# Kernel optimization log

Measured on AMD Instinct MI355X. Metric: run time of the kernel, lower is better.

The kernel has to match this reference:

```python
import jax, jax.numpy as jnp
import numpy as np

SIZE = 256
D_IN = 256
EPS = 1e-3  # keras BatchNormalization default epsilon


def _mlp(x, W1, b1, W2, b2):
    # smallMLP: Dense(size, relu) -> Dense(size)
    return jax.nn.relu(x @ W1 + b1) @ W2 + b2


def setup_inputs() -> dict:
    key = jax.random.key(0)
    ks = jax.random.split(key, 20)
    B, L1, L2 = 16, 1024, 1024
    s = 0.02
    inp = {
        "seq1M": jax.random.normal(ks[0], (B, L1, D_IN), jnp.float32),
        "seq2M": jax.random.normal(ks[1], (B, L2, D_IN), jnp.float32),
        "distogram": jax.random.uniform(ks[2], (B, L1, L2), jnp.float32),
        # shared K/Q/V smallMLP params (same layers applied to seq1 and seq2)
        "kW1": jax.random.normal(ks[3], (D_IN, SIZE), jnp.float32) * s,
        "kb1": jnp.zeros((SIZE,), jnp.float32),
        "kW2": jax.random.normal(ks[4], (SIZE, SIZE), jnp.float32) * s,
        "kb2": jnp.zeros((SIZE,), jnp.float32),
        "qW1": jax.random.normal(ks[5], (D_IN, SIZE), jnp.float32) * s,
        "qb1": jnp.zeros((SIZE,), jnp.float32),
        "qW2": jax.random.normal(ks[6], (SIZE, SIZE), jnp.float32) * s,
        "qb2": jnp.zeros((SIZE,), jnp.float32),
        "vW1": jax.random.normal(ks[7], (D_IN, SIZE), jnp.float32) * s,
        "vb1": jnp.zeros((SIZE,), jnp.float32),
        "vW2": jax.random.normal(ks[8], (SIZE, SIZE), jnp.float32) * s,
        "vb2": jnp.zeros((SIZE,), jnp.float32),
        # output projections
        "fc1W": jax.random.normal(ks[9], (SIZE, SIZE), jnp.float32) * s,
        "fc1b": jnp.zeros((SIZE,), jnp.float32),
        "fc2W": jax.random.normal(ks[10], (SIZE, SIZE), jnp.float32) * s,
        "fc2b": jnp.zeros((SIZE,), jnp.float32),
        # shared BatchNorm (inference mode, moving stats)
        "bn_gamma": jnp.ones((SIZE,), jnp.float32),
        "bn_beta": jnp.zeros((SIZE,), jnp.float32),
        "bn_mean": jnp.zeros((SIZE,), jnp.float32),
        "bn_var": jnp.ones((SIZE,), jnp.float32),
    }
    return inp


def reference(seq1M, seq2M, distogram,
              kW1, kb1, kW2, kb2,
              qW1, qb1, qW2, qb2,
              vW1, vb1, vW2, vb2,
              fc1W, fc1b, fc2W, fc2b,
              bn_gamma, bn_beta, bn_mean, bn_var):
    size = jnp.float32(SIZE)
    k1 = _mlp(seq1M, kW1, kb1, kW2, kb2)   # [B, L1, S]
    q1 = _mlp(seq1M, qW1, qb1, qW2, qb2)
    v1 = _mlp(seq1M, vW1, vb1, vW2, vb2)
    k2 = _mlp(seq2M, kW1, kb1, kW2, kb2)   # [B, L2, S]
    q2 = _mlp(seq2M, qW1, qb1, qW2, qb2)
    v2 = _mlp(seq2M, vW1, vb1, vW2, vb2)

    # distogram-scaled scores, softmax over axis 1 (query axis — non-standard)
    scores1 = jnp.einsum('bls,bms->blm', q1, k2) * distogram / size  # [B, L1, L2]
    w1 = jax.nn.softmax(scores1, axis=1)
    scores2 = jnp.einsum('bms,bls->bml', q2, k1) * jnp.transpose(distogram, (0, 2, 1)) / size  # [B, L2, L1]
    w2 = jax.nn.softmax(scores2, axis=1)

    # transpose(matmul(V^T, W), [0,2,1]) == einsum contracting the softmax axis
    ap1 = jnp.einsum('bls,blm->bms', v1, w1)  # [B, L2, S]
    ap2 = jnp.einsum('bms,bml->bls', v2, w2)  # [B, L1, S]

    def bn(x):
        return (x - bn_mean) * jax.lax.rsqrt(bn_var + EPS) * bn_gamma + bn_beta

    out1 = bn(jax.nn.relu(ap1 @ fc1W + fc1b))
    out2 = bn(jax.nn.relu(ap2 @ fc2W + fc2b))
    return out1, out2
```

## Files before the change

### kernel.cpp

```cpp
#include <hip/hip_runtime.h>
#include <hip/hip_bf16.h>


typedef __attribute__((ext_vector_type(8))) short bf16x8;
typedef __attribute__((ext_vector_type(4))) float f32x4;
typedef unsigned short u16;

__device__ __forceinline__ unsigned int f2bfbits(float f) {
  union { float f; unsigned int i; } v; v.f = f;
  return (v.i + 0x7fffu + ((v.i >> 16) & 1u)) >> 16;
}
__device__ __forceinline__ unsigned int pk2(float a, float b) {
  return f2bfbits(a) | (f2bfbits(b) << 16);
}
__device__ __forceinline__ float bf2f(u16 x) {
  union { unsigned int i; float f; } v;
  v.i = (unsigned int)x << 16;
  return v.f;
}

__global__ void pack_wt(const float* __restrict__ w0, const float* __restrict__ w1,
                        const float* __restrict__ w2, const float* __restrict__ w3,
                        const float* __restrict__ w4, const float* __restrict__ w5,
                        const float* __restrict__ w6, const float* __restrict__ w7,
                        u16* __restrict__ out) {
  const float* wsel[8] = {w0, w1, w2, w3, w4, w5, w6, w7};
  const float* W = wsel[blockIdx.y];
  u16* o = out + (size_t)blockIdx.y * 65536;
  int i0 = blockIdx.x * 1024 + threadIdx.x * 4;
  int n = i0 >> 8, k = i0 & 255;
  float a = W[(k + 0) * 256 + n];
  float b = W[(k + 1) * 256 + n];
  float c = W[(k + 2) * 256 + n];
  float d = W[(k + 3) * 256 + n];
  uint2 pv;
  pv.x = pk2(a, b);
  pv.y = pk2(c, d);
  *(uint2*)(o + i0) = pv;
}

__global__ __launch_bounds__(256, 2)
void mlp3_plus(const float* __restrict__ seqA, const float* __restrict__ seqB,
               const u16* __restrict__ Wt8,
               const float* __restrict__ kb1, const float* __restrict__ kb2,
               const float* __restrict__ qb1, const float* __restrict__ qb2,
               const float* __restrict__ vb1, const float* __restrict__ vb2,
               u16* __restrict__ kA, u16* __restrict__ qA, u16* __restrict__ vA,
               u16* __restrict__ kB, u16* __restrict__ qB, u16* __restrict__ vB,
               const float* __restrict__ D, u16* __restrict__ Dt)
{
  __shared__ union {
    struct {
      u16 As[64][256];
      u16 Hl[64][256];
    } m;
    u16 T[64][72];
  } sh;

  const int tid = threadIdx.x;

  if (blockIdx.x >= 512) {
    const int pb = blockIdx.x - 512;
    const int m0 = (pb & 15) * 64;
    const int l0 = ((pb >> 4) & 15) * 64;
    const int b = pb >> 8;
    const float* src = D + (size_t)b * (1024 * 1024);
    u16* dst = Dt + (size_t)b * (1024 * 1024);
    const int r = tid >> 2, c0 = (tid & 3) * 16;
    float4 f[4];
#pragma unroll
    for (int q = 0; q < 4; ++q)
      f[q] = *(const float4*)(src + (size_t)(l0 + r) * 1024 + m0 + c0 + q * 4);
    uint4 p0, p1;
    p0.x = pk2(f[0].x, f[0].y); p0.y = pk2(f[0].z, f[0].w);
    p0.z = pk2(f[1].x, f[1].y); p0.w = pk2(f[1].z, f[1].w);
    p1.x = pk2(f[2].x, f[2].y); p1.y = pk2(f[2].z, f[2].w);
    p1.z = pk2(f[3].x, f[3].y); p1.w = pk2(f[3].z, f[3].w);
    *(uint4*)&sh.T[r][c0] = p0;
    *(uint4*)&sh.T[r][c0 + 8] = p1;
    __syncthreads();
    u16 vals[16];
#pragma unroll
    for (int k = 0; k < 16; ++k) vals[k] = sh.T[c0 + k][r];
    *(uint4*)(dst + (size_t)(m0 + r) * 1024 + l0 + c0) = *(uint4*)&vals[0];
    *(uint4*)(dst + (size_t)(m0 + r) * 1024 + l0 + c0 + 8) = *(uint4*)&vals[8];
    return;
  }

  const int lane = tid & 63;
  const int w = tid >> 6;
  const int l15 = lane & 15, lq = lane >> 4;
  const int seqsel = blockIdx.x >> 8;
  const size_t m0 = (size_t)(blockIdx.x & 255) * 64;
  const float* __restrict__ seq = seqsel ? seqB : seqA;

  {
    const int row = tid >> 2, cg = tid & 3;
    const float* src = seq + (m0 + row) * 256 + cg * 64;
#pragma unroll
    for (int cc = 0; cc < 8; ++cc) {
      float4 f0 = *(const float4*)(src + cc * 8);
      float4 f1 = *(const float4*)(src + cc * 8 + 4);
      uint4 pk;
      pk.x = pk2(f0.x, f0.y);
      pk.y = pk2(f0.z, f0.w);
      pk.z = pk2(f1.x, f1.y);
      pk.w = pk2(f1.z, f1.w);
      const int ch = (cg * 8 + cc) ^ (row & 7);
      *(uint4*)&sh.m.As[row][ch * 8] = pk;
    }
  }
  __syncthreads();

  for (int mlp = 0; mlp < 3; ++mlp) {
    const u16* __restrict__ W1 = Wt8 + (size_t)(mlp * 2) * 65536;
    const u16* __restrict__ W2 = W1 + 65536;
    const float* __restrict__ b1 = (mlp == 0) ? kb1 : (mlp == 1) ? qb1 : vb1;
    const float* __restrict__ b2 = (mlp == 0) ? kb2 : (mlp == 1) ? qb2 : vb2;
    u16* __restrict__ dst =
        (mlp == 0) ? (seqsel ? kB : kA) : (mlp == 1) ? (seqsel ? qB : qA) : (seqsel ? vB : vA);

    const u16* __restrict__ w1b = W1 + (size_t)(w * 64 + l15) * 256 + lq * 8;
    const u16* __restrict__ w2b = W2 + (size_t)(w * 64 + l15) * 256 + lq * 8;

    bf16x8 wf[3][4];
#pragma unroll
    for (int ni = 0; ni < 4; ++ni) wf[0][ni] = *(const bf16x8*)(w1b + ni * 4096);
#pragma unroll
    for (int ni = 0; ni < 4; ++ni) wf[1][ni] = *(const bf16x8*)(w1b + ni * 4096 + 32);

    float b1v[4][4];
#pragma unroll
    for (int ni = 0; ni < 4; ++ni)
#pragma unroll
      for (int r = 0; r < 4; ++r) b1v[ni][r] = b1[w * 64 + ni * 16 + 4 * lq + r];
    float b2v[4];
#pragma unroll
    for (int ni = 0; ni < 4; ++ni) b2v[ni] = b2[w * 64 + ni * 16 + l15];

    f32x4 a1[4][4];
#pragma unroll
    for (int ni = 0; ni < 4; ++ni)
#pragma unroll
      for (int mj = 0; mj < 4; ++mj) a1[ni][mj] = (f32x4)0.0f;
#pragma unroll
    for (int ks = 0; ks < 8; ++ks) {
      if (ks + 2 < 8) {
#pragma unroll
        for (int ni = 0; ni < 4; ++ni)
          wf[(ks + 2) % 3][ni] = *(const bf16x8*)(w1b + ni * 4096 + (ks + 2) * 32);
      }
      bf16x8 af[4];
#pragma unroll
      for (int mj = 0; mj < 4; ++mj) {
        const int row = mj * 16 + l15;
        const int ch = (ks * 4 + lq) ^ (row & 7);
        af[mj] = *(const bf16x8*)&sh.m.As[row][ch * 8];
      }
#pragma unroll
      for (int ni = 0; ni < 4; ++ni)
#pragma unroll
        for (int mj = 0; mj < 4; ++mj)
          a1[ni][mj] = __builtin_amdgcn_mfma_f32_16x16x32_bf16(
              wf[ks % 3][ni], af[mj], a1[ni][mj], 0, 0, 0);
    }

    __syncthreads();

#pragma unroll
    for (int ni = 0; ni < 4; ++ni) wf[0][ni] = *(const bf16x8*)(w2b + ni * 4096);
#pragma unroll
    for (int ni = 0; ni < 4; ++ni) wf[1][ni] = *(const bf16x8*)(w2b + ni * 4096 + 32);

#pragma unroll
    for (int ni = 0; ni < 4; ++ni) {
      const int chl = w * 8 + ni * 2 + (lq >> 1);
#pragma unroll
      for (int mj = 0; mj < 4; ++mj) {
        const int m = mj * 16 + l15;
        float h0 = fmaxf(a1[ni][mj][0] + b1v[ni][0], 0.f);
        float h1 = fmaxf(a1[ni][mj][1] + b1v[ni][1], 0.f);
        float h2 = fmaxf(a1[ni][mj][2] + b1v[ni][2], 0.f);
        float h3 = fmaxf(a1[ni][mj][3] + b1v[ni][3], 0.f);
        uint2 pv;
        pv.x = pk2(h0, h1);
        pv.y = pk2(h2, h3);
        const int ch = chl ^ (m & 7);
        *(uint2*)&sh.m.Hl[m][ch * 8 + (lq & 1) * 4] = pv;
      }
    }
    __syncthreads();

    f32x4 a2[4][4];
#pragma unroll
    for (int mi = 0; mi < 4; ++mi)
#pragma unroll
      for (int ni = 0; ni < 4; ++ni) a2[mi][ni] = (f32x4)0.0f;
#pragma unroll
    for (int ks = 0; ks < 8; ++ks) {
      if (ks + 2 < 8) {
#pragma unroll
        for (int ni = 0; ni < 4; ++ni)
          wf[(ks + 2) % 3][ni] = *(const bf16x8*)(w2b + ni * 4096 + (ks + 2) * 32);
      }
      bf16x8 hf[4];
#pragma unroll
      for (int mi = 0; mi < 4; ++mi) {
        const int row = mi * 16 + l15;
        const int ch = (ks * 4 + lq) ^ (row & 7);
        hf[mi] = *(const bf16x8*)&sh.m.Hl[row][ch * 8];
      }
#pragma unroll
      for (int mi = 0; mi < 4; ++mi)
#pragma unroll
        for (int ni = 0; ni < 4; ++ni)
          a2[mi][ni] = __builtin_amdgcn_mfma_f32_16x16x32_bf16(
              hf[mi], wf[ks % 3][ni], a2[mi][ni], 0, 0, 0);
    }

#pragma unroll
    for (int ni = 0; ni < 4; ++ni) {
      const int col = w * 64 + ni * 16 + l15;
      const float bb = b2v[ni];
#pragma unroll
      for (int mi = 0; mi < 4; ++mi) {
        const size_t grow0 = m0 + mi * 16 + 4 * lq;
        float z[4];
#pragma unroll
        for (int r = 0; r < 4; ++r) z[r] = a2[mi][ni][r] + bb;
        if (mlp != 2) {
#pragma unroll
          for (int r = 0; r < 4; ++r)
            dst[(grow0 + r) * 256 + col] = (u16)f2bfbits(z[r]);
        } else {
          uint2 pv;
          pv.x = pk2(z[0], z[1]);
          pv.y = pk2(z[2], z[3]);
          const size_t bb2 = grow0 >> 10, lrow = grow0 & 1023;
          *(uint2*)(dst + ((size_t)bb2 * 256 + col) * 1024 + lrow) = pv;
        }
      }
    }
  }
}

__global__ __launch_bounds__(256, 2)
void gemm_bn2(const u16* __restrict__ ap1, const u16* __restrict__ ap2,
              const u16* __restrict__ Wt8,
              const float* __restrict__ fc1b, const float* __restrict__ fc2b,
              float* __restrict__ out1, float* __restrict__ out2,
              const float* __restrict__ bn_g, const float* __restrict__ bn_b,
              const float* __restrict__ bn_m, const float* __restrict__ bn_v)
{
  __shared__ u16 As[128][64];
  __shared__ u16 Ws[64][64];
  const int tid = threadIdx.x;
  const int lane = tid & 63;
  const int w = tid >> 6;
  const int wr = w >> 1, wc = w & 1;
  const int l15 = lane & 15, lq = lane >> 4;
  const size_t bm = (size_t)blockIdx.x * 128;
  const int bn = blockIdx.y * 64;
  const int which = blockIdx.z;

  const u16* __restrict__ A0 = which ? ap2 : ap1;
  const u16* __restrict__ Wt = Wt8 + (size_t)(6 + which) * 65536;
  const float* __restrict__ bias = which ? fc2b : fc1b;
  float* __restrict__ Cout = which ? out2 : out1;

  const int sar = tid >> 1, sah = tid & 1;
  const int swr = tid >> 2, swc = tid & 3;

  f32x4 acc[4][2];
#pragma unroll
  for (int mi = 0; mi < 4; ++mi)
#pragma unroll
    for (int ni = 0; ni < 2; ++ni) acc[mi][ni] = (f32x4)0.0f;

  for (int k0 = 0; k0 < 256; k0 += 64) {
    __syncthreads();
    {
      const u16* A = A0 + (bm + sar) * 256 + k0 + sah * 32;
#pragma unroll
      for (int c = 0; c < 4; ++c) {
        uint4 v = *(const uint4*)(A + c * 8);
        int cc = (sah * 4 + c) ^ (sar & 7);
        *(uint4*)&As[sar][cc * 8] = v;
      }
    }
    {
      const u16* Wp = Wt + (size_t)(bn + swr) * 256 + k0 + swc * 16;
#pragma unroll
      for (int c = 0; c < 2; ++c) {
        uint4 v = *(const uint4*)(Wp + c * 8);
        int cc = (swc * 2 + c) ^ (swr & 7);
        *(uint4*)&Ws[swr][cc * 8] = v;
      }
    }
    __syncthreads();
#pragma unroll
    for (int ks = 0; ks < 2; ++ks) {
      bf16x8 af[4], wf[2];
#pragma unroll
      for (int mi = 0; mi < 4; ++mi) {
        int row = wr * 64 + mi * 16 + l15;
        int cc = (ks * 4 + lq) ^ (row & 7);
        af[mi] = *(const bf16x8*)&As[row][cc * 8];
      }
#pragma unroll
      for (int ni = 0; ni < 2; ++ni) {
        int row = wc * 32 + ni * 16 + l15;
        int cc = (ks * 4 + lq) ^ (row & 7);
        wf[ni] = *(const bf16x8*)&Ws[row][cc * 8];
      }
#pragma unroll
      for (int mi = 0; mi < 4; ++mi)
#pragma unroll
        for (int ni = 0; ni < 2; ++ni)
          acc[mi][ni] = __builtin_amdgcn_mfma_f32_16x16x32_bf16(
              af[mi], wf[ni], acc[mi][ni], 0, 0, 0);
    }
  }

#pragma unroll
  for (int ni = 0; ni < 2; ++ni) {
    const int col = bn + wc * 32 + ni * 16 + l15;
    const float bi = bias[col];
    const float g = bn_g[col];
    const float be = bn_b[col];
    const float mu = bn_m[col];
    const float iv = rsqrtf(bn_v[col] + 1e-3f);
#pragma unroll
    for (int mi = 0; mi < 4; ++mi) {
      const size_t grow0 = bm + wr * 64 + mi * 16 + 4 * lq;
#pragma unroll
      for (int r = 0; r < 4; ++r) {
        float z = acc[mi][ni][r] + bi;
        float zz = fmaxf(z, 0.f);
        Cout[(grow0 + r) * 256 + col] = (zz - mu) * iv * g + be;
      }
    }
  }
}

__global__ __launch_bounds__(512, 2)
void attn_mfma(const u16* __restrict__ Qa, const u16* __restrict__ Ka,
               const u16* __restrict__ Va, u16* __restrict__ OutA,
               const u16* __restrict__ Qb, const u16* __restrict__ Kb,
               const u16* __restrict__ Vb, u16* __restrict__ OutB,
               const u16* __restrict__ D1t, const float* __restrict__ D2)
{
  __shared__ union U {
    struct {
      u16 Ks[2][64][256];
      u16 Vts[2][256][64];
      u16 Pl[128][72];
    } s;
    u16 Osw[8][16][264];
  } u;

  const int orig = blockIdx.x;
  const int lid = (orig & 7) * 32 + (orig >> 3);
  const int dir = lid >> 7;
  const int b = (lid >> 3) & 15;
  const int i0 = (lid & 7) * 128;

  const u16* __restrict__ Q = dir ? Qb : Qa;
  const u16* __restrict__ K = dir ? Kb : Ka;
  const u16* __restrict__ Vt = dir ? Vb : Va;
  u16* __restrict__ Out = dir ? OutB : OutA;

  const int tid = threadIdx.x;
  const int lane = tid & 63;
  const int w = tid >> 6;
  const int l15 = lane & 15, lq = lane >> 4;
  const size_t sbase = (size_t)b * (1024 * 256);
  const size_t vtbase = (size_t)b * (256 * 1024);
  const size_t dbase = (size_t)b * (1024 * 1024);

  bf16x8 q[8];
  {
    const u16* Qp = Q + sbase + (size_t)(i0 + w * 16 + l15) * 256 + lq * 8;
#pragma unroll
    for (int ks = 0; ks < 8; ++ks) q[ks] = *(const bf16x8*)(Qp + ks * 32);
  }

  const int cb0 = w * 4;
  auto stage_K = [&](int bi, int j0) {
#pragma unroll
    for (int i = 0; i < 4; ++i) {
      const int cb = cb0 + i;
      const int krow = cb * 2 + (lane >> 5);
      const int kch = (lane & 31) ^ (krow & 7);
      const u16* gs = K + sbase + (size_t)(j0 + krow) * 256 + kch * 8;
      __builtin_amdgcn_global_load_lds(
          (const __attribute__((address_space(1))) unsigned int*)gs,
          (__attribute__((address_space(3))) unsigned int*)&u.s.Ks[bi][cb * 2][0],
          16, 0, 0);
    }
  };
  auto stage_V = [&](int bi, int j0) {
#pragma unroll
    for (int i = 0; i < 4; ++i) {
      const int cb = cb0 + i;
      const int vrow = cb * 8 + (lane >> 3);
      const int vch = lane & 7;
      const u16* gs = Vt + vtbase + (size_t)vrow * 1024 + j0 + ((vch ^ (vrow & 7)) * 8);
      __builtin_amdgcn_global_load_lds(
          (const __attribute__((address_space(1))) unsigned int*)gs,
          (__attribute__((address_space(3))) unsigned int*)&u.s.Vts[bi][cb * 8][0],
          16, 0, 0);
    }
  };

  float mrow[4], lsum[4];
  f32x4 o[16];
#pragma unroll
  for (int r = 0; r < 4; ++r) { mrow[r] = -1e30f; lsum[r] = 0.f; }
#pragma unroll
  for (int nt = 0; nt < 16; ++nt) o[nt] = (f32x4)0.0f;

  stage_K(0, 0);
  stage_V(0, 0);

  for (int t = 0; t < 16; ++t) {
    const int bi = t & 1;
    const int j0 = t * 64;

    u16 bregu[16];
    float bregf[16];
    if (dir == 0) {
#pragma unroll
      for (int nt = 0; nt < 4; ++nt)
#pragma unroll
        for (int r = 0; r < 4; ++r)
          bregu[nt * 4 + r] =
              D1t[dbase + (size_t)(i0 + w * 16 + 4 * lq + r) * 1024 + j0 + l15 + 16 * nt];
    } else {
#pragma unroll
      for (int nt = 0; nt < 4; ++nt)
#pragma unroll
        for (int r = 0; r < 4; ++r)
          bregf[nt * 4 + r] =
              D2[dbase + (size_t)(i0 + w * 16 + 4 * lq + r) * 1024 + j0 + l15 + 16 * nt];
    }

    if (t + 1 < 16) {
      stage_V(bi ^ 1, j0 + 64);
      stage_K(bi ^ 1, j0 + 64);
      asm volatile("s_waitcnt vmcnt(24)" ::: "memory");
    } else {
      asm volatile("s_waitcnt vmcnt(16)" ::: "memory");
    }
    __builtin_amdgcn_s_barrier();
    __builtin_amdgcn_sched_barrier(0);

    f32x4 sa[4];
#pragma unroll
    for (int nt = 0; nt < 4; ++nt) sa[nt] = (f32x4)0.0f;
    __builtin_amdgcn_s_setprio(1);
#pragma unroll
    for (int ks = 0; ks < 8; ++ks)
#pragma unroll
      for (int nt = 0; nt < 4; ++nt) {
        const int row = nt * 16 + l15;
        const int cc = (ks * 4 + lq) ^ (row & 7);
        bf16x8 kb = *(const bf16x8*)&u.s.Ks[bi][row][cc * 8];
        sa[nt] = __builtin_amdgcn_mfma_f32_16x16x32_bf16(q[ks], kb, sa[nt], 0, 0, 0);
      }
    __builtin_amdgcn_s_setprio(0);

    float s[4][4];
    bool need = false;
#pragma unroll
    for (int r = 0; r < 4; ++r)
#pragma unroll
      for (int nt = 0; nt < 4; ++nt) {
        const float bb = (dir == 0) ? bf2f(bregu[nt * 4 + r]) : bregf[nt * 4 + r];
        s[r][nt] = sa[nt][r] * bb * 0.00390625f;
        need = need || (s[r][nt] > mrow[r] + 8.f);
      }
    if (__any(need)) {
#pragma unroll
      for (int r = 0; r < 4; ++r) {
        float mx = fmaxf(fmaxf(s[r][0], s[r][1]), fmaxf(s[r][2], s[r][3]));
        mx = fmaxf(mx, __shfl_xor(mx, 1, 16));
        mx = fmaxf(mx, __shfl_xor(mx, 2, 16));
        mx = fmaxf(mx, __shfl_xor(mx, 4, 16));
        mx = fmaxf(mx, __shfl_xor(mx, 8, 16));
        const float mn = fmaxf(mrow[r], mx);
        const float sc = __expf(mrow[r] - mn);
        mrow[r] = mn;
        lsum[r] *= sc;
#pragma unroll
        for (int nt = 0; nt < 16; ++nt) o[nt][r] *= sc;
      }
    }
#pragma unroll
    for (int r = 0; r < 4; ++r) {
      const int qrow = w * 16 + 4 * lq + r;
#pragma unroll
      for (int nt = 0; nt < 4; ++nt) {
        const float p = __expf(s[r][nt] - mrow[r]);
        lsum[r] += p;
        u.s.Pl[qrow][nt * 16 + l15] = (u16)f2bfbits(p);
      }
    }
    asm volatile("s_waitcnt lgkmcnt(0)" ::: "memory");
    __builtin_amdgcn_sched_barrier(0);
    const bf16x8 pa0 = *(const bf16x8*)&u.s.Pl[w * 16 + l15][lq * 8];
    const bf16x8 pa1 = *(const bf16x8*)&u.s.Pl[w * 16 + l15][32 + lq * 8];

    __builtin_amdgcn_s_setprio(1);
#pragma unroll
    for (int nt = 0; nt < 16; ++nt) {
      const int row = nt * 16 + l15;
      const int cc0 = (0 * 4 + lq) ^ (row & 7);
      const int cc1 = (1 * 4 + lq) ^ (row & 7);
      bf16x8 vb0 = *(const bf16x8*)&u.s.Vts[bi][row][cc0 * 8];
      bf16x8 vb1 = *(const bf16x8*)&u.s.Vts[bi][row][cc1 * 8];
      o[nt] = __builtin_amdgcn_mfma_f32_16x16x32_bf16(pa0, vb0, o[nt], 0, 0, 0);
      o[nt] = __builtin_amdgcn_mfma_f32_16x16x32_bf16(pa1, vb1, o[nt], 0, 0, 0);
    }
    __builtin_amdgcn_s_setprio(0);

    asm volatile("s_waitcnt lgkmcnt(0)" ::: "memory");
    __builtin_amdgcn_s_barrier();
  }

  float inv[4];
#pragma unroll
  for (int r = 0; r < 4; ++r) {
    float rs = lsum[r];
    rs += __shfl_xor(rs, 1, 16);
    rs += __shfl_xor(rs, 2, 16);
    rs += __shfl_xor(rs, 4, 16);
    rs += __shfl_xor(rs, 8, 16);
    inv[r] = 1.0f / rs;
  }
  __builtin_amdgcn_s_barrier();
#pragma unroll
  for (int nt = 0; nt < 16; ++nt) {
#pragma unroll
    for (int r = 0; r < 4; ++r)
      u.Osw[w][4 * lq + r][nt * 16 + l15] = (u16)f2bfbits(o[nt][r] * inv[r]);
  }
  asm volatile("s_waitcnt lgkmcnt(0)" ::: "memory");
  __builtin_amdgcn_sched_barrier(0);
  {
    const int orow = lane >> 2, och = (lane & 3) * 64;
    const u16* src = &u.Osw[w][orow][och];
    u16* dst = Out + sbase + (size_t)(i0 + w * 16 + orow) * 256 + och;
#pragma unroll
    for (int c = 0; c < 8; ++c) *(uint4*)(dst + c * 8) = *(const uint4*)(src + c * 8);
  }
}

extern "C" void kernel_launch(void* const* d_in, const int* in_sizes, int n_in,
                              void* d_out, int out_size, void* d_ws, size_t ws_size,
                              hipStream_t stream)
{
  (void)in_sizes; (void)n_in; (void)out_size; (void)ws_size;

  const float* seq1  = (const float*)d_in[0];
  const float* seq2  = (const float*)d_in[1];
  const float* disto = (const float*)d_in[2];
  const float* kW1 = (const float*)d_in[3];
  const float* kb1 = (const float*)d_in[4];
  const float* kW2 = (const float*)d_in[5];
  const float* kb2 = (const float*)d_in[6];
  const float* qW1 = (const float*)d_in[7];
  const float* qb1 = (const float*)d_in[8];
  const float* qW2 = (const float*)d_in[9];
  const float* qb2 = (const float*)d_in[10];
  const float* vW1 = (const float*)d_in[11];
  const float* vb1 = (const float*)d_in[12];
  const float* vW2 = (const float*)d_in[13];
  const float* vb2 = (const float*)d_in[14];
  const float* fc1W = (const float*)d_in[15];
  const float* fc1b = (const float*)d_in[16];
  const float* fc2W = (const float*)d_in[17];
  const float* fc2b = (const float*)d_in[18];
  const float* bn_g = (const float*)d_in[19];
  const float* bn_b = (const float*)d_in[20];
  const float* bn_m = (const float*)d_in[21];
  const float* bn_v = (const float*)d_in[22];

  char* ws = (char*)d_ws;
  const size_t MB = 1024 * 1024;
  u16* Wt8 = (u16*)(ws);
  u16* k1  = (u16*)(ws + 1 * MB);
  u16* q1  = (u16*)(ws + 9 * MB);
  u16* k2  = (u16*)(ws + 17 * MB);
  u16* q2  = (u16*)(ws + 25 * MB);
  u16* v1t = (u16*)(ws + 33 * MB);
  u16* v2t = (u16*)(ws + 41 * MB);
  u16* ap1 = (u16*)(ws + 49 * MB);
  u16* ap2 = (u16*)(ws + 57 * MB);
  u16* D1t = (u16*)(ws + 65 * MB);

  pack_wt<<<dim3(64, 8), 256, 0, stream>>>(kW1, kW2, qW1, qW2, vW1, vW2, fc1W, fc2W, Wt8);

  mlp3_plus<<<dim3(4608), dim3(256), 0, stream>>>(
      seq1, seq2, Wt8, kb1, kb2, qb1, qb2, vb1, vb2,
      k1, q1, v1t, k2, q2, v2t, disto, D1t);

  attn_mfma<<<dim3(256), dim3(512), 0, stream>>>(
      k2, q1, v1t, ap1,
      k1, q2, v2t, ap2,
      D1t, disto);

  float* out1 = (float*)d_out;
  float* out2 = (float*)d_out + 4194304;
  gemm_bn2<<<dim3(128, 4, 2), dim3(256), 0, stream>>>(
      ap1, ap2, Wt8, fc1b, fc2b, out1, out2, bn_g, bn_b, bn_m, bn_v);
}
```

Before: 161.3 us.

## Fuse output FC projection, ReLU and BatchNorm into attention kernel epilogue

Removes the separate gemm_bn2 kernel. Each attention warp now reads its normalized 16x256 output tile from LDS as MFMA A-fragments and multiplies it by the FC weight matrix, loaded straight from global memory with one-step register prefetch. It then applies bias, ReLU and BatchNorm and writes fp32 results directly. This drops the bf16 ap1/ap2 round trip through memory and one kernel launch. In exchange, the attention kernel's tail gets longer, every warp reloads the full 256x256 weights from global/L2 without LDS sharing, and register pressure rises.

```diff
diff --git a/kernel.cpp b/kernel.cpp
--- a/kernel.cpp
+++ b/kernel.cpp
@@ -244,111 +244,17 @@
   }
 }
 
-__global__ __launch_bounds__(256, 2)
-void gemm_bn2(const u16* __restrict__ ap1, const u16* __restrict__ ap2,
-              const u16* __restrict__ Wt8,
-              const float* __restrict__ fc1b, const float* __restrict__ fc2b,
-              float* __restrict__ out1, float* __restrict__ out2,
-              const float* __restrict__ bn_g, const float* __restrict__ bn_b,
-              const float* __restrict__ bn_m, const float* __restrict__ bn_v)
-{
-  __shared__ u16 As[128][64];
-  __shared__ u16 Ws[64][64];
-  const int tid = threadIdx.x;
-  const int lane = tid & 63;
-  const int w = tid >> 6;
-  const int wr = w >> 1, wc = w & 1;
-  const int l15 = lane & 15, lq = lane >> 4;
-  const size_t bm = (size_t)blockIdx.x * 128;
-  const int bn = blockIdx.y * 64;
-  const int which = blockIdx.z;
-
-  const u16* __restrict__ A0 = which ? ap2 : ap1;
-  const u16* __restrict__ Wt = Wt8 + (size_t)(6 + which) * 65536;
-  const float* __restrict__ bias = which ? fc2b : fc1b;
-  float* __restrict__ Cout = which ? out2 : out1;
-
-  const int sar = tid >> 1, sah = tid & 1;
-  const int swr = tid >> 2, swc = tid & 3;
-
-  f32x4 acc[4][2];
-#pragma unroll
-  for (int mi = 0; mi < 4; ++mi)
-#pragma unroll
-    for (int ni = 0; ni < 2; ++ni) acc[mi][ni] = (f32x4)0.0f;
-
-  for (int k0 = 0; k0 < 256; k0 += 64) {
-    __syncthreads();
-    {
-      const u16* A = A0 + (bm + sar) * 256 + k0 + sah * 32;
-#pragma unroll
-      for (int c = 0; c < 4; ++c) {
-        uint4 v = *(const uint4*)(A + c * 8);
-        int cc = (sah * 4 + c) ^ (sar & 7);
-        *(uint4*)&As[sar][cc * 8] = v;
-      }
-    }
-    {
-      const u16* Wp = Wt + (size_t)(bn + swr) * 256 + k0 + swc * 16;
-#pragma unroll
-      for (int c = 0; c < 2; ++c) {
-        uint4 v = *(const uint4*)(Wp + c * 8);
-        int cc = (swc * 2 + c) ^ (swr & 7);
-        *(uint4*)&Ws[swr][cc * 8] = v;
-      }
-    }
-    __syncthreads();
-#pragma unroll
-    for (int ks = 0; ks < 2; ++ks) {
-      bf16x8 af[4], wf[2];
-#pragma unroll
-      for (int mi = 0; mi < 4; ++mi) {
-        int row = wr * 64 + mi * 16 + l15;
-        int cc = (ks * 4 + lq) ^ (row & 7);
-        af[mi] = *(const bf16x8*)&As[row][cc * 8];
-      }
-#pragma unroll
-      for (int ni = 0; ni < 2; ++ni) {
-        int row = wc * 32 + ni * 16 + l15;
-        int cc = (ks * 4 + lq) ^ (row & 7);
-        wf[ni] = *(const bf16x8*)&Ws[row][cc * 8];
-      }
-#pragma unroll
-      for (int mi = 0; mi < 4; ++mi)
-#pragma unroll
-        for (int ni = 0; ni < 2; ++ni)
-          acc[mi][ni] = __builtin_amdgcn_mfma_f32_16x16x32_bf16(
-              af[mi], wf[ni], acc[mi][ni], 0, 0, 0);
-    }
-  }
-
-#pragma unroll
-  for (int ni = 0; ni < 2; ++ni) {
-    const int col = bn + wc * 32 + ni * 16 + l15;
-    const float bi = bias[col];
-    const float g = bn_g[col];
-    const float be = bn_b[col];
-    const float mu = bn_m[col];
-    const float iv = rsqrtf(bn_v[col] + 1e-3f);
-#pragma unroll
-    for (int mi = 0; mi < 4; ++mi) {
-      const size_t grow0 = bm + wr * 64 + mi * 16 + 4 * lq;
-#pragma unroll
-      for (int r = 0; r < 4; ++r) {
-        float z = acc[mi][ni][r] + bi;
-        float zz = fmaxf(z, 0.f);
-        Cout[(grow0 + r) * 256 + col] = (zz - mu) * iv * g + be;
-      }
-    }
-  }
-}
-
 __global__ __launch_bounds__(512, 2)
 void attn_mfma(const u16* __restrict__ Qa, const u16* __restrict__ Ka,
-               const u16* __restrict__ Va, u16* __restrict__ OutA,
+               const u16* __restrict__ Va,
                const u16* __restrict__ Qb, const u16* __restrict__ Kb,
-               const u16* __restrict__ Vb, u16* __restrict__ OutB,
-               const u16* __restrict__ D1t, const float* __restrict__ D2)
+               const u16* __restrict__ Vb,
+               const u16* __restrict__ D1t, const float* __restrict__ D2,
+               const u16* __restrict__ WtFC,
+               const float* __restrict__ fc1b, const float* __restrict__ fc2b,
+               float* __restrict__ out1, float* __restrict__ out2,
+               const float* __restrict__ bn_g, const float* __restrict__ bn_b,
+               const float* __restrict__ bn_m, const float* __restrict__ bn_v)
 {
   __shared__ union U {
     struct {
@@ -368,7 +274,6 @@
   const u16* __restrict__ Q = dir ? Qb : Qa;
   const u16* __restrict__ K = dir ? Kb : Ka;
   const u16* __restrict__ Vt = dir ? Vb : Va;
-  u16* __restrict__ Out = dir ? OutB : OutA;
 
   const int tid = threadIdx.x;
   const int lane = tid & 63;
@@ -547,12 +452,57 @@
   }
   asm volatile("s_waitcnt lgkmcnt(0)" ::: "memory");
   __builtin_amdgcn_sched_barrier(0);
-  {
-    const int orow = lane >> 2, och = (lane & 3) * 64;
-    const u16* src = &u.Osw[w][orow][och];
-    u16* dst = Out + sbase + (size_t)(i0 + w * 16 + orow) * 256 + och;
-#pragma unroll
-    for (int c = 0; c < 8; ++c) *(uint4*)(dst + c * 8) = *(const uint4*)(src + c * 8);
+
+  bf16x8 afv[8];
+#pragma unroll
+  for (int ks = 0; ks < 8; ++ks)
+    afv[ks] = *(const bf16x8*)&u.Osw[w][l15][ks * 32 + lq * 8];
+
+  const u16* __restrict__ Wt = WtFC + (size_t)dir * 65536;
+  const float* __restrict__ fcb = dir ? fc2b : fc1b;
+  float* __restrict__ Cout = dir ? out2 : out1;
+  const u16* __restrict__ wfb = Wt + (size_t)l15 * 256 + lq * 8;
+
+#pragma unroll
+  for (int nc = 0; nc < 4; ++nc) {
+    f32x4 acc[4];
+#pragma unroll
+    for (int ni = 0; ni < 4; ++ni) acc[ni] = (f32x4)0.0f;
+    bf16x8 wf[4], wn[4];
+#pragma unroll
+    for (int ni = 0; ni < 4; ++ni)
+      wf[ni] = *(const bf16x8*)(wfb + (size_t)(nc * 64 + ni * 16) * 256);
+#pragma unroll
+    for (int ks = 0; ks < 8; ++ks) {
+      if (ks < 7) {
+#pragma unroll
+        for (int ni = 0; ni < 4; ++ni)
+          wn[ni] = *(const bf16x8*)(wfb + (size_t)(nc * 64 + ni * 16) * 256 + (ks + 1) * 32);
+      }
+#pragma unroll
+      for (int ni = 0; ni < 4; ++ni)
+        acc[ni] = __builtin_amdgcn_mfma_f32_16x16x32_bf16(afv[ks], wf[ni], acc[ni], 0, 0, 0);
+#pragma unroll
+      for (int ni = 0; ni < 4; ++ni) wf[ni] = wn[ni];
+    }
+#pragma unroll
+    for (int ni = 0; ni < 4; ++ni) {
+      const int col = nc * 64 + ni * 16 + l15;
+      const float bi = fcb[col];
+      const float g = bn_g[col];
+      const float be = bn_b[col];
+      const float mu = bn_m[col];
+      const float iv = rsqrtf(bn_v[col] + 1e-3f);
+      const size_t grow0 = sbase / 256 * 256;
+      (void)grow0;
+      const size_t row0 = (size_t)b * 1024 + i0 + w * 16 + 4 * lq;
+#pragma unroll
+      for (int r = 0; r < 4; ++r) {
+        float z = acc[ni][r] + bi;
+        float zz = fmaxf(z, 0.f);
+        Cout[(row0 + r) * 256 + col] = (zz - mu) * iv * g + be;
+      }
+    }
   }
 }
 
@@ -595,8 +545,6 @@
   u16* q2  = (u16*)(ws + 25 * MB);
   u16* v1t = (u16*)(ws + 33 * MB);
   u16* v2t = (u16*)(ws + 41 * MB);
-  u16* ap1 = (u16*)(ws + 49 * MB);
-  u16* ap2 = (u16*)(ws + 57 * MB);
   u16* D1t = (u16*)(ws + 65 * MB);
 
   pack_wt<<<dim3(64, 8), 256, 0, stream>>>(kW1, kW2, qW1, qW2, vW1, vW2, fc1W, fc2W, Wt8);
@@ -605,13 +553,12 @@
       seq1, seq2, Wt8, kb1, kb2, qb1, qb2, vb1, vb2,
       k1, q1, v1t, k2, q2, v2t, disto, D1t);
 
-  attn_mfma<<<dim3(256), dim3(512), 0, stream>>>(
-      k2, q1, v1t, ap1,
-      k1, q2, v2t, ap2,
-      D1t, disto);
-
   float* out1 = (float*)d_out;
   float* out2 = (float*)d_out + 4194304;
-  gemm_bn2<<<dim3(128, 4, 2), dim3(256), 0, stream>>>(
-      ap1, ap2, Wt8, fc1b, fc2b, out1, out2, bn_g, bn_b, bn_m, bn_v);
-}
+  attn_mfma<<<dim3(256), dim3(512), 0, stream>>>(
+      k2, q1, v1t,
+      k1, q2, v2t,
+      D1t, disto,
+      Wt8 + 6ull * 65536, fc1b, fc2b, out1, out2,
+      bn_g, bn_b, bn_m, bn_v);
+}
```

Result: slower. 175.9 us (+9.0%).
